# Kernel tuning notes

Measured on AMD Instinct MI355X. Metric: run time of the kernel, lower is better.

Reference implementation:

```python
import jax, jax.numpy as jnp
import numpy as np

VOCAB, EMB, HID, L = 100000, 128, 256, 9
B, S = 128, 512
H = HID // 2  # per-direction hidden size
PAD = 0


def setup_inputs() -> dict:
    key = jax.random.key(0)
    ks = jax.random.split(key, 18)
    seqs = jax.random.randint(ks[0], (B, S), 1, VOCAB)
    # left-aligned padding: lengths in [S//2, S]
    lens = jax.random.randint(ks[1], (B,), S // 2, S + 1)
    seqs = jnp.where(jnp.arange(S)[None, :] < lens[:, None], seqs, PAD)
    labels = jax.random.randint(ks[2], (B, S), 0, L)

    def n(k, shape, s=0.05):
        return jax.random.normal(k, shape, jnp.float32) * s

    emb = n(ks[3], (VOCAB, EMB)).at[PAD].set(0.0)
    inp = {
        'sequences': seqs, 'labels': labels, 'emb': emb,
        'w_ih_f': n(ks[4], (4 * H, EMB)), 'w_hh_f': n(ks[5], (4 * H, H)),
        'b_ih_f': n(ks[6], (4 * H,)), 'b_hh_f': n(ks[7], (4 * H,)),
        'w_ih_b': n(ks[8], (4 * H, EMB)), 'w_hh_b': n(ks[9], (4 * H, H)),
        'b_ih_b': n(ks[10], (4 * H,)), 'b_hh_b': n(ks[11], (4 * H,)),
        'w_out': n(ks[12], (L, HID)), 'b_out': n(ks[13], (L,)),
        'start_t': n(ks[14], (L,), 0.1), 'end_t': n(ks[15], (L,), 0.1),
        'trans': n(ks[16], (L, L), 0.1),
    }
    return inp


def _lstm_scan(x, w_ih, w_hh, b_ih, b_hh):
    # x: [S, B, E] -> hidden states [S, B, H]
    h0 = jnp.zeros((x.shape[1], w_hh.shape[1]), x.dtype)

    def step(carry, xt):
        h, c = carry
        g = xt @ w_ih.T + b_ih + h @ w_hh.T + b_hh
        i, f, gg, o = jnp.split(g, 4, axis=-1)  # PyTorch gate order i,f,g,o
        c = jax.nn.sigmoid(f) * c + jax.nn.sigmoid(i) * jnp.tanh(gg)
        h = jax.nn.sigmoid(o) * jnp.tanh(c)
        return (h, c), h

    _, hs = jax.lax.scan(step, (h0, h0), x)
    return hs


def reference(sequences, labels, emb, w_ih_f, w_hh_f, b_ih_f, b_hh_f,
              w_ih_b, w_hh_b, b_ih_b, b_hh_b, w_out, b_out,
              start_t, end_t, trans):
    # Embedding lookup (dropout is identity at inference)
    x = emb[sequences]                      # [B,S,E]
    xt = jnp.swapaxes(x, 0, 1)              # [S,B,E]
    hf = _lstm_scan(xt, w_ih_f, w_hh_f, b_ih_f, b_hh_f)
    hb = _lstm_scan(xt[::-1], w_ih_b, w_hh_b, b_ih_b, b_hh_b)[::-1]
    hcat = jnp.concatenate([hf, hb], axis=-1)         # [S,B,HID]
    emissions = jnp.swapaxes(hcat, 0, 1) @ w_out.T + b_out  # [B,S,L]

    mask = sequences != PAD                 # [B,S], first step all True
    maskf = mask.astype(emissions.dtype)

    # --- CRF numerator (score of gold path) ---
    em_tag = jnp.take_along_axis(emissions, labels[..., None], axis=2)[..., 0]  # [B,S]
    trans_sc = trans[labels[:, :-1], labels[:, 1:]]                              # [B,S-1]
    num = start_t[labels[:, 0]] + em_tag[:, 0] \
        + jnp.sum((trans_sc + em_tag[:, 1:]) * maskf[:, 1:], axis=1)
    seq_ends = jnp.sum(mask, axis=1) - 1
    last_tags = labels[jnp.arange(labels.shape[0]), seq_ends]
    num = num + end_t[last_tags]

    # --- CRF partition function (forward algorithm) ---
    def fstep(score, inp):
        em_t, m_t = inp  # [B,L], [B]
        nxt = jax.nn.logsumexp(score[:, :, None] + trans[None] + em_t[:, None, :], axis=1)
        return jnp.where(m_t[:, None], nxt, score), None

    score0 = start_t[None, :] + emissions[:, 0]  # [B,L]
    em_rest = jnp.swapaxes(emissions, 0, 1)[1:]  # [S-1,B,L]
    scoreT, _ = jax.lax.scan(fstep, score0, (em_rest, mask.T[1:]))
    denom = jax.nn.logsumexp(scoreT + end_t[None, :], axis=1)  # [B]

    # model returns -log_likelihood (torchcrf default reduction='sum')
    return -jnp.sum(num - denom)
```

## Files before the change

### kernel.cpp

```cpp
#include <hip/hip_runtime.h>
#include <hip/hip_bf16.h>

#define B_   128
#define S_   512
#define H_   128
#define G_   512
#define EMB_ 128
#define NL_  9

typedef __attribute__((ext_vector_type(8))) short bf16x8;
typedef __attribute__((ext_vector_type(4))) short bf16x4;
typedef __attribute__((ext_vector_type(4))) float f32x4;
typedef unsigned short ushort_t;

__device__ __forceinline__ void wg_bar() {
    asm volatile("s_waitcnt lgkmcnt(0)\n\ts_barrier" ::: "memory");
}

__device__ __forceinline__ float bfbits2f(short s) {
    unsigned int u = ((unsigned int)(unsigned short)s) << 16;
    return __builtin_bit_cast(float, u);
}
__device__ __forceinline__ short f2bf(float f) {
    unsigned int u = __builtin_bit_cast(unsigned int, f);
    u += 0x7FFFu + ((u >> 16) & 1u);
    return (short)(u >> 16);
}
__device__ __forceinline__ unsigned int pack2(float lo, float hi) {
    return (unsigned int)(unsigned short)f2bf(lo) | ((unsigned int)(unsigned short)f2bf(hi) << 16);
}
__device__ __forceinline__ float exp2_(float x) {
    float r;
    asm("v_exp_f32 %0, %1" : "=v"(r) : "v"(x));
    return r;
}
__device__ __forceinline__ float sigm(float x) {
    return __builtin_amdgcn_rcpf(1.f + exp2_(-1.4426950408889634f * x));
}
__device__ __forceinline__ float tanh_(float x) {
    return 1.f - 2.f * __builtin_amdgcn_rcpf(1.f + exp2_(2.8853900817779268f * x));
}

__global__ __launch_bounds__(512, 1)
void xw_gemm_kernel(const int* __restrict__ seq, const float* __restrict__ emb,
                    const float* __restrict__ w_ih_f, const float* __restrict__ b_ih_f,
                    const float* __restrict__ b_hh_f,
                    const float* __restrict__ w_ih_b, const float* __restrict__ b_ih_b,
                    const float* __restrict__ b_hh_b,
                    ushort_t* __restrict__ xw)
{
    __shared__ bf16x8 ldsX[64 * 17];

    const int tid  = threadIdx.x;
    const int wv   = tid >> 6;
    const int n16  = tid & 15;
    const int quad = (tid & 63) >> 4;
    const int dir  = blockIdx.x >> 10;
    const int rem  = blockIdx.x & 1023;
    const int pair = rem >> 4;
    const int tb   = (rem & 15) * 32;

    const float* wih = dir ? w_ih_b : w_ih_f;
    const float* bih = dir ? b_ih_b : b_ih_f;
    const float* bhh = dir ? b_hh_b : b_hh_f;

    {
        int row = tid >> 3, part = tid & 7;
        int b = 2 * pair + (row >> 5);
        int t = tb + (row & 31);
        int tok = seq[b * S_ + t];
        const float* ep = emb + (size_t)tok * EMB_ + part * 16;
        int rt = row >> 4, rr = row & 15;
#pragma unroll
        for (int h = 0; h < 2; h++) {
            float4 a = *(const float4*)(ep + h * 8);
            float4 b4 = *(const float4*)(ep + h * 8 + 4);
            bf16x8 fr;
            fr[0] = f2bf(a.x); fr[1] = f2bf(a.y); fr[2] = f2bf(a.z); fr[3] = f2bf(a.w);
            fr[4] = f2bf(b4.x); fr[5] = f2bf(b4.y); fr[6] = f2bf(b4.z); fr[7] = f2bf(b4.w);
            ldsX[(rt * 16 + part * 2 + h) * 17 + rr] = fr;
        }
    }

    bf16x8 bfrag[4][4];
    float  bias[4];
#pragma unroll
    for (int nt = 0; nt < 4; nt++) {
        int col = nt * 128 + wv * 16 + n16;
        bias[nt] = bih[col] + bhh[col];
#pragma unroll
        for (int ks = 0; ks < 4; ks++) {
            const float* p = wih + col * EMB_ + ks * 32 + quad * 8;
            bf16x8 fr;
#pragma unroll
            for (int j = 0; j < 8; j++) fr[j] = f2bf(p[j]);
            bfrag[nt][ks] = fr;
        }
    }
    __syncthreads();

    const size_t plane0 = (size_t)(dir * 128 + 2 * pair);

#pragma unroll
    for (int half = 0; half < 2; half++) {
        f32x4 accA[4], accB[4];
        bf16x8 afA[4], afB[4];
#pragma unroll
        for (int ks = 0; ks < 4; ks++) {
            afA[ks] = ldsX[(half * 16 + ks * 4 + quad) * 17 + n16];
            afB[ks] = ldsX[((half + 2) * 16 + ks * 4 + quad) * 17 + n16];
        }
#pragma unroll
        for (int nt = 0; nt < 4; nt++) {
            f32x4 a = {bias[nt], bias[nt], bias[nt], bias[nt]};
            accA[nt] = a; accB[nt] = a;
#pragma unroll
            for (int ks = 0; ks < 4; ks++) {
                accA[nt] = __builtin_amdgcn_mfma_f32_16x16x32_bf16(afA[ks], bfrag[nt][ks], accA[nt], 0, 0, 0);
                accB[nt] = __builtin_amdgcn_mfma_f32_16x16x32_bf16(afB[ks], bfrag[nt][ks], accB[nt], 0, 0, 0);
            }
        }
        const int u = wv * 16 + n16;
#pragma unroll
        for (int r = 0; r < 4; r++) {
            int t = tb + half * 16 + quad * 4 + r;
            int2 iv0, iv1;
            iv0.x = (int)pack2(accA[0][r], accA[1][r]);
            iv0.y = (int)pack2(accA[2][r], accA[3][r]);
            iv1.x = (int)pack2(accB[0][r], accB[1][r]);
            iv1.y = (int)pack2(accB[2][r], accB[3][r]);
            *(int2*)(xw + ((plane0 * S_ + t) * 128 + u) * 4) = iv0;
            *(int2*)(xw + (((plane0 + 1) * S_ + t) * 128 + u) * 4) = iv1;
        }
    }
}

#define STEPK(k)                                                                   \
  {                                                                                \
    if ((k) == 0 && s4 == 0 && m < 31) {                                           \
      const ushort_t* gp = xwp + (size_t)(dir ? (S_ - 32 - m16) : (m16 + 16)) * 512; \
      sA = *(const int4*)(gp + tid * 8);                                           \
      sB = *(const int4*)(gp + 2048 + tid * 8);                                    \
      sC = *(const int4*)(gp + 4096 + tid * 8);                                    \
      sD = *(const int4*)(gp + 6144 + tid * 8);                                    \
    }                                                                              \
    bf16x8 af0 = hbuf[(k) & 1][0 * 4 + quad];                                      \
    bf16x8 af1 = hbuf[(k) & 1][1 * 4 + quad];                                      \
    bf16x8 af2 = hbuf[(k) & 1][2 * 4 + quad];                                      \
    bf16x8 af3 = hbuf[(k) & 1][3 * 4 + quad];                                      \
    const int KE = s4x4 + (k);                                                     \
    const int slot = dir ? (15 - KE) : KE;                                         \
    bf16x4 xvg = *(const bf16x4*)(xwS + (m & 1) * 8192 + slot * 512 + uu * 4);     \
    if ((k) == 0 && s4 == 2 && m < 31) {                                           \
      int4* dst = (int4*)(xwL + (((m & 1) ^ 1) * 1024));                           \
      dst[tid] = sA; dst[256 + tid] = sB; dst[512 + tid] = sC; dst[768 + tid] = sD; \
    }                                                                              \
    if ((k) == 1 && s4 == 0 && m >= 1 && wv == 3 && lane < 36) {                   \
      int a0 = dir ? (S_ - m16) : (m16 - 16);                                      \
      float4 fv = *(const float4*)(emL + (a0 & 31) * 9 + lane * 4);                \
      *(float4*)(emdir + (size_t)b * (S_ * NL_) + a0 * NL_ + lane * 4) = fv;       \
    }                                                                              \
    f32x4 aA0 = __builtin_amdgcn_mfma_f32_16x16x32_bf16(af0, bfrag[0][0][0], ZACC, 0, 0, 0); \
    f32x4 aA1 = __builtin_amdgcn_mfma_f32_16x16x32_bf16(af0, bfrag[0][1][0], ZACC, 0, 0, 0); \
    f32x4 aA2 = __builtin_amdgcn_mfma_f32_16x16x32_bf16(af0, bfrag[0][2][0], ZACC, 0, 0, 0); \
    f32x4 aA3 = __builtin_amdgcn_mfma_f32_16x16x32_bf16(af0, bfrag[0][3][0], ZACC, 0, 0, 0); \
    f32x4 aB0 = __builtin_amdgcn_mfma_f32_16x16x32_bf16(af0, bfrag[1][0][0], ZACC, 0, 0, 0); \
    f32x4 aB1 = __builtin_amdgcn_mfma_f32_16x16x32_bf16(af0, bfrag[1][1][0], ZACC, 0, 0, 0); \
    f32x4 aB2 = __builtin_amdgcn_mfma_f32_16x16x32_bf16(af0, bfrag[1][2][0], ZACC, 0, 0, 0); \
    f32x4 aB3 = __builtin_amdgcn_mfma_f32_16x16x32_bf16(af0, bfrag[1][3][0], ZACC, 0, 0, 0); \
    aA0 = __builtin_amdgcn_mfma_f32_16x16x32_bf16(af1, bfrag[0][0][1], aA0, 0, 0, 0); \
    aA1 = __builtin_amdgcn_mfma_f32_16x16x32_bf16(af1, bfrag[0][1][1], aA1, 0, 0, 0); \
    aA2 = __builtin_amdgcn_mfma_f32_16x16x32_bf16(af1, bfrag[0][2][1], aA2, 0, 0, 0); \
    aA3 = __builtin_amdgcn_mfma_f32_16x16x32_bf16(af1, bfrag[0][3][1], aA3, 0, 0, 0); \
    aB0 = __builtin_amdgcn_mfma_f32_16x16x32_bf16(af1, bfrag[1][0][1], aB0, 0, 0, 0); \
    aB1 = __builtin_amdgcn_mfma_f32_16x16x32_bf16(af1, bfrag[1][1][1], aB1, 0, 0, 0); \
    aB2 = __builtin_amdgcn_mfma_f32_16x16x32_bf16(af1, bfrag[1][2][1], aB2, 0, 0, 0); \
    aB3 = __builtin_amdgcn_mfma_f32_16x16x32_bf16(af1, bfrag[1][3][1], aB3, 0, 0, 0); \
    aA0 = __builtin_amdgcn_mfma_f32_16x16x32_bf16(af2, bfrag[0][0][2], aA0, 0, 0, 0); \
    aA1 = __builtin_amdgcn_mfma_f32_16x16x32_bf16(af2, bfrag[0][1][2], aA1, 0, 0, 0); \
    aA2 = __builtin_amdgcn_mfma_f32_16x16x32_bf16(af2, bfrag[0][2][2], aA2, 0, 0, 0); \
    aA3 = __builtin_amdgcn_mfma_f32_16x16x32_bf16(af2, bfrag[0][3][2], aA3, 0, 0, 0); \
    aB0 = __builtin_amdgcn_mfma_f32_16x16x32_bf16(af2, bfrag[1][0][2], aB0, 0, 0, 0); \
    aB1 = __builtin_amdgcn_mfma_f32_16x16x32_bf16(af2, bfrag[1][1][2], aB1, 0, 0, 0); \
    aB2 = __builtin_amdgcn_mfma_f32_16x16x32_bf16(af2, bfrag[1][2][2], aB2, 0, 0, 0); \
    aB3 = __builtin_amdgcn_mfma_f32_16x16x32_bf16(af2, bfrag[1][3][2], aB3, 0, 0, 0); \
    aA0 = __builtin_amdgcn_mfma_f32_16x16x32_bf16(af3, bfrag[0][0][3], aA0, 0, 0, 0); \
    aA1 = __builtin_amdgcn_mfma_f32_16x16x32_bf16(af3, bfrag[0][1][3], aA1, 0, 0, 0); \
    aA2 = __builtin_amdgcn_mfma_f32_16x16x32_bf16(af3, bfrag[0][2][3], aA2, 0, 0, 0); \
    aA3 = __builtin_amdgcn_mfma_f32_16x16x32_bf16(af3, bfrag[0][3][3], aA3, 0, 0, 0); \
    aB0 = __builtin_amdgcn_mfma_f32_16x16x32_bf16(af3, bfrag[1][0][3], aB0, 0, 0, 0); \
    aB1 = __builtin_amdgcn_mfma_f32_16x16x32_bf16(af3, bfrag[1][1][3], aB1, 0, 0, 0); \
    aB2 = __builtin_amdgcn_mfma_f32_16x16x32_bf16(af3, bfrag[1][2][3], aB2, 0, 0, 0); \
    aB3 = __builtin_amdgcn_mfma_f32_16x16x32_bf16(af3, bfrag[1][3][3], aB3, 0, 0, 0); \
    {                                                                              \
      float gi = ((quad & 2) ? aB0[0] : aA0[0]) + bfbits2f(xvg[0]);                \
      float gf = ((quad & 2) ? aB1[0] : aA1[0]) + bfbits2f(xvg[1]);                \
      float gg = ((quad & 2) ? aB2[0] : aA2[0]) + bfbits2f(xvg[2]);                \
      float go = ((quad & 2) ? aB3[0] : aA3[0]) + bfbits2f(xvg[3]);                \
      float Af = exp2_(-1.4426950408889634f * gf);                                 \
      float Bi = exp2_(-1.4426950408889634f * gi);                                 \
      float Cg = exp2_(2.8853900817779268f * gg);                                  \
      float Fo = exp2_(-1.4426950408889634f * go);                                 \
      float oA = 1.f + Af, oB = 1.f + Bi, oC = 1.f + Cg;                           \
      float P = oB * oC;                                                           \
      float numer = cst * P + oA * (Cg - 1.f);                                     \
      cst = numer * __builtin_amdgcn_rcpf(oA * P);                                 \
      float hv = tanh_(cst) * __builtin_amdgcn_rcpf(1.f + Fo);                     \
      if (!(quad & 1)) *(((k) & 1) ? hw0 : hw1) = f2bf(hv);                        \
    }                                                                              \
    if (wv == 0) {                                                                 \
      f32x4 accE = __builtin_amdgcn_mfma_f32_16x16x32_bf16(af0, bfragE[0], ZACC, 0, 0, 0); \
      accE = __builtin_amdgcn_mfma_f32_16x16x32_bf16(af1, bfragE[1], accE, 0, 0, 0); \
      accE = __builtin_amdgcn_mfma_f32_16x16x32_bf16(af2, bfragE[2], accE, 0, 0, 0); \
      accE = __builtin_amdgcn_mfma_f32_16x16x32_bf16(af3, bfragE[3], accE, 0, 0, 0); \
      if (quad == 0 && n16 < NL_ && (m16 + KE) >= 1) {                             \
        int tprev = dir ? (S_ - (m16 + KE)) : (m16 + KE - 1);                      \
        emL[(tprev & 31) * 9 + n16] = accE[0];                                     \
      }                                                                            \
    }                                                                              \
    wg_bar();                                                                      \
  }

__global__ __launch_bounds__(256, 1)
void lstm_kernel(const ushort_t* __restrict__ xw,
                 const float* __restrict__ w_hh_f, const float* __restrict__ w_hh_b,
                 const float* __restrict__ w_out,
                 float* __restrict__ em_f, float* __restrict__ em_b)
{
    __shared__ bf16x8 xwL[2 * 1024];
    __shared__ bf16x8 hbuf[2][16];
    __shared__ __align__(16) float emL[32 * NL_];

    const int tid  = threadIdx.x;
    const int wv   = tid >> 6;
    const int lane = tid & 63;
    const int n16  = tid & 15;
    const int quad = (tid & 63) >> 4;
    const int dir  = blockIdx.x >> 7;
    const int b    = blockIdx.x & 127;

    const int uu = wv * 32 + ((quad >> 1) << 4) + n16;

    short* hw0 = ((short*)hbuf) + uu;
    short* hw1 = ((short*)hbuf) + 128 + uu;
    const short* xwS = (const short*)xwL;

    const f32x4 ZACC = {0.f, 0.f, 0.f, 0.f};

    const float* whh = dir ? w_hh_b : w_hh_f;
    float* emdir = dir ? em_b : em_f;

    bf16x8 bfrag[2][4][4];
#pragma unroll
    for (int tl = 0; tl < 2; tl++) {
#pragma unroll
        for (int nt = 0; nt < 4; nt++) {
            int col = nt * 128 + wv * 32 + tl * 16 + n16;
#pragma unroll
            for (int ks = 0; ks < 4; ks++) {
                const float* p = whh + col * H_ + ks * 32 + quad * 8;
                bf16x8 fr;
#pragma unroll
                for (int j = 0; j < 8; j++) fr[j] = f2bf(p[j]);
                bfrag[tl][nt][ks] = fr;
            }
        }
    }
    bf16x8 bfragE[4];
#pragma unroll
    for (int ks = 0; ks < 4; ks++) {
        bf16x8 fr = {0, 0, 0, 0, 0, 0, 0, 0};
        if (n16 < NL_) {
            const float* p = w_out + n16 * 256 + dir * 128 + ks * 32 + quad * 8;
#pragma unroll
            for (int j = 0; j < 8; j++) fr[j] = f2bf(p[j]);
        }
        bfragE[ks] = fr;
    }

    if (tid < 64) ((int*)hbuf)[tid] = 0;

    const ushort_t* xwp = xw + (size_t)(dir * 128 + b) * ((size_t)S_ * 512);
    {
        const ushort_t* gp = xwp + (size_t)(dir ? (S_ - 16) : 0) * 512;
        int4 a0 = *(const int4*)(gp + tid * 8);
        int4 a1 = *(const int4*)(gp + 2048 + tid * 8);
        int4 a2 = *(const int4*)(gp + 4096 + tid * 8);
        int4 a3 = *(const int4*)(gp + 6144 + tid * 8);
        int4* dst = (int4*)xwL;
        dst[tid] = a0; dst[256 + tid] = a1; dst[512 + tid] = a2; dst[768 + tid] = a3;
    }

    float cst = 0.f;
    int4 sA, sB, sC, sD;
    wg_bar();

#pragma unroll 1
    for (int m = 0; m < 32; m++) {
        const int m16 = m << 4;
#pragma unroll 1
        for (int s4 = 0; s4 < 4; s4++) {
            const int s4x4 = s4 << 2;
            STEPK(0) STEPK(1) STEPK(2) STEPK(3)
        }
    }

    if (wv == 0) {
        bf16x8 af0 = hbuf[0][0 * 4 + quad];
        bf16x8 af1 = hbuf[0][1 * 4 + quad];
        bf16x8 af2 = hbuf[0][2 * 4 + quad];
        bf16x8 af3 = hbuf[0][3 * 4 + quad];
        f32x4 accE = __builtin_amdgcn_mfma_f32_16x16x32_bf16(af0, bfragE[0], ZACC, 0, 0, 0);
        accE = __builtin_amdgcn_mfma_f32_16x16x32_bf16(af1, bfragE[1], accE, 0, 0, 0);
        accE = __builtin_amdgcn_mfma_f32_16x16x32_bf16(af2, bfragE[2], accE, 0, 0, 0);
        accE = __builtin_amdgcn_mfma_f32_16x16x32_bf16(af3, bfragE[3], accE, 0, 0, 0);
        if (quad == 0 && n16 < NL_) {
            int tprev = dir ? 0 : (S_ - 1);
            emL[(tprev & 31) * 9 + n16] = accE[0];
        }
    }
    wg_bar();
    if (wv == 3 && lane < 36) {
        int a0 = dir ? 0 : (S_ - 16);
        float4 fv = *(const float4*)(emL + (a0 & 31) * 9 + lane * 4);
        *(float4*)(emdir + (size_t)b * (S_ * NL_) + a0 * NL_ + lane * 4) = fv;
    }
}

__global__ __launch_bounds__(640, 1)
void crf_kernel(const int* __restrict__ seq, const int* __restrict__ lab,
                const float* __restrict__ em_f, const float* __restrict__ em_b,
                const float* __restrict__ b_out,
                const float* __restrict__ start_t, const float* __restrict__ end_t,
                const float* __restrict__ trans, float* __restrict__ partial)
{
    __shared__ float emS[S_ * NL_];
    __shared__ float transS[NL_ * NL_];
    __shared__ float stS[NL_], enS[NL_];
    __shared__ unsigned char maskS[S_];
    __shared__ float MS[7 * 81];
    __shared__ float vS[NL_];
    __shared__ float redw[10];
    __shared__ int   redl[10];

    const int b = blockIdx.x, tid = threadIdx.x;
    const size_t base = (size_t)b * S_ * NL_;
    const float L2E = 1.4426950408889634f, LN2 = 0.6931471805599453f;

    for (int q = tid; q < S_ * NL_; q += 640)
        emS[q] = em_f[base + q] + em_b[base + q] + b_out[q % NL_];
    if (tid < NL_ * NL_) transS[tid] = trans[tid];
    if (tid < NL_) { stS[tid] = start_t[tid]; enS[tid] = end_t[tid]; }
    if (tid < S_) maskS[tid] = (seq[b * S_ + tid] != 0);
    __syncthreads();

    float np = 0.f; int myc = 0;
    if (tid < S_) {
        myc = maskS[tid];
        if (tid >= 1 && maskS[tid]) {
            int lp = lab[b * S_ + tid - 1], lc = lab[b * S_ + tid];
            np = transS[lp * NL_ + lc] + emS[tid * NL_ + lc];
        }
    }
#pragma unroll
    for (int off = 32; off; off >>= 1) {
        np  += __shfl_down(np, off, 64);
        myc += __shfl_down(myc, off, 64);
    }
    if ((tid & 63) == 0) { redw[tid >> 6] = np; redl[tid >> 6] = myc; }

    const int w = tid >> 6, l = tid & 63;
    const int lg = l / 9;
    const int g  = w * 7 + lg;
    const bool sact = (lg < 7) && (g < 64);
    const int jj = sact ? (l - lg * 9) : 0;
    const int gb = sact ? lg * 9 : 0;
    float Tc[NL_];
#pragma unroll
    for (int i = 0; i < NL_; i++) Tc[i] = transS[i * NL_ + jj];
    float sc; int tbeg, tend, cN = 0, iN = 0;
    if (sact && g == 0) {
        sc = stS[jj] + emS[jj];
        tbeg = 1; tend = 64;
    } else if (sact) {
        cN = 1 + (g - 1) / 9; iN = (g - 1) % 9;
        sc = (jj == iN) ? 0.f : -1e30f;
        tbeg = cN * 64; tend = tbeg + 64;
    } else {
        sc = -1e30f; tbeg = 448; tend = 512;
    }
    for (int t = tbeg; t < tend; t++) {
        float emv = emS[t * NL_ + jj];
        float a[NL_];
#pragma unroll
        for (int i = 0; i < NL_; i++) a[i] = __shfl(sc, gb + i, 64) + Tc[i];
        float m = a[0];
#pragma unroll
        for (int i = 1; i < NL_; i++) m = fmaxf(m, a[i]);
        float sum = 0.f;
#pragma unroll
        for (int i = 0; i < NL_; i++) sum += exp2f((a[i] - m) * L2E);
        float nxt = emv + m + LN2 * log2f(sum);
        sc = maskS[t] ? nxt : sc;
    }
    if (sact) {
        if (g == 0) vS[jj] = sc;
        else MS[(cN - 1) * 81 + iN * NL_ + jj] = sc;
    }
    __syncthreads();

    if (tid < 64) {
        const int j = (tid < NL_) ? tid : (NL_ - 1);
        float v = vS[j];
        for (int c = 1; c < 8; c++) {
            float a[NL_];
#pragma unroll
            for (int i = 0; i < NL_; i++)
                a[i] = __shfl(v, i, 64) + MS[(c - 1) * 81 + i * NL_ + j];
            float m = a[0];
#pragma unroll
            for (int i = 1; i < NL_; i++) m = fmaxf(m, a[i]);
            float sum = 0.f;
#pragma unroll
            for (int i = 0; i < NL_; i++) sum += exp2f((a[i] - m) * L2E);
            v = m + LN2 * log2f(sum);
        }
        v += enS[j];
        float mm = -1e30f, av[NL_];
#pragma unroll
        for (int i = 0; i < NL_; i++) { float vi = __shfl(v, i, 64); av[i] = vi; mm = fmaxf(mm, vi); }
        float ss = 0.f;
#pragma unroll
        for (int i = 0; i < NL_; i++) ss += exp2f((av[i] - mm) * L2E);
        if (tid == 0) {
            float num = 0.f; int len = 0;
#pragma unroll
            for (int ww = 0; ww < 10; ww++) { num += redw[ww]; len += redl[ww]; }
            int l0 = lab[b * S_];
            int ll = lab[b * S_ + len - 1];
            num += stS[l0] + emS[l0] + enS[ll];
            partial[b] = (mm + LN2 * log2f(ss)) - num;
        }
    }
}

__global__ __launch_bounds__(128)
void reduce_kernel(const float* __restrict__ partial, float* __restrict__ out)
{
    __shared__ float s[128];
    int tid = threadIdx.x;
    s[tid] = partial[tid];
    __syncthreads();
    for (int off = 64; off; off >>= 1) {
        if (tid < off) s[tid] += s[tid + off];
        __syncthreads();
    }
    if (tid == 0) out[0] = s[0];
}

extern "C" void kernel_launch(void* const* d_in, const int* in_sizes, int n_in,
                              void* d_out, int out_size, void* d_ws, size_t ws_size,
                              hipStream_t stream)
{
    const int* seq = (const int*)d_in[0];
    const int* lab = (const int*)d_in[1];
    const float* emb    = (const float*)d_in[2];
    const float* w_ih_f = (const float*)d_in[3];
    const float* w_hh_f = (const float*)d_in[4];
    const float* b_ih_f = (const float*)d_in[5];
    const float* b_hh_f = (const float*)d_in[6];
    const float* w_ih_b = (const float*)d_in[7];
    const float* w_hh_b = (const float*)d_in[8];
    const float* b_ih_b = (const float*)d_in[9];
    const float* b_hh_b = (const float*)d_in[10];
    const float* w_out  = (const float*)d_in[11];
    const float* b_out  = (const float*)d_in[12];
    const float* start_t = (const float*)d_in[13];
    const float* end_t   = (const float*)d_in[14];
    const float* trans   = (const float*)d_in[15];

    char* ws = (char*)d_ws;
    const size_t xw_bytes = (size_t)2 * B_ * S_ * G_ * sizeof(ushort_t);
    const size_t em_bytes = (size_t)B_ * S_ * NL_ * sizeof(float);
    ushort_t* xw   = (ushort_t*)ws;
    float* em_f    = (float*)(ws + xw_bytes);
    float* em_b    = (float*)(ws + xw_bytes + em_bytes);
    float* partial = (float*)(ws + xw_bytes + 2 * em_bytes);

    xw_gemm_kernel<<<dim3(2048), dim3(512), 0, stream>>>(seq, emb,
        w_ih_f, b_ih_f, b_hh_f, w_ih_b, b_ih_b, b_hh_b, xw);
    lstm_kernel<<<dim3(256), dim3(256), 0, stream>>>(xw, w_hh_f, w_hh_b,
        w_out, em_f, em_b);
    crf_kernel<<<dim3(B_), dim3(640), 0, stream>>>(seq, lab, em_f, em_b, b_out,
        start_t, end_t, trans, partial);
    reduce_kernel<<<dim3(1), dim3(128), 0, stream>>>(partial, (float*)d_out);
}
```

Before: 497.4 us.

## Fuse input-projection GEMM into LSTM recurrence kernel, drop xw workspace

Removes the separate xw_gemm kernel and its large bf16 workspace. Each LSTM workgroup now gathers the embeddings for the next 16 timesteps, converts them to bf16 and runs a small MFMA GEMM against register-resident W_ih fragments, writing into the LDS staging buffer in the slots of the recurrence steps. This cuts the global write and read of the input-projection tensor and one launch. The cost is many more registers held across the recurrent loop and extra MFMA work on the serial critical path. The CRF logsumexp also switches to v_max3, raw v_exp/v_log and tree sums.

```diff
diff --git a/kernel.cpp b/kernel.cpp
--- a/kernel.cpp
+++ b/kernel.cpp
@@ -30,119 +30,64 @@
     return (unsigned int)(unsigned short)f2bf(lo) | ((unsigned int)(unsigned short)f2bf(hi) << 16);
 }
 __device__ __forceinline__ float exp2_(float x) {
-    float r;
-    asm("v_exp_f32 %0, %1" : "=v"(r) : "v"(x));
-    return r;
-}
-__device__ __forceinline__ float sigm(float x) {
-    return __builtin_amdgcn_rcpf(1.f + exp2_(-1.4426950408889634f * x));
+    float r; asm("v_exp_f32 %0, %1" : "=v"(r) : "v"(x)); return r;
+}
+__device__ __forceinline__ float log2_(float x) {
+    float r; asm("v_log_f32 %0, %1" : "=v"(r) : "v"(x)); return r;
+}
+__device__ __forceinline__ float max3_(float a, float b, float c) {
+    float r; asm("v_max3_f32 %0, %1, %2, %3" : "=v"(r) : "v"(a), "v"(b), "v"(c)); return r;
 }
 __device__ __forceinline__ float tanh_(float x) {
     return 1.f - 2.f * __builtin_amdgcn_rcpf(1.f + exp2_(2.8853900817779268f * x));
 }
-
-__global__ __launch_bounds__(512, 1)
-void xw_gemm_kernel(const int* __restrict__ seq, const float* __restrict__ emb,
-                    const float* __restrict__ w_ih_f, const float* __restrict__ b_ih_f,
-                    const float* __restrict__ b_hh_f,
-                    const float* __restrict__ w_ih_b, const float* __restrict__ b_ih_b,
-                    const float* __restrict__ b_hh_b,
-                    ushort_t* __restrict__ xw)
-{
-    __shared__ bf16x8 ldsX[64 * 17];
-
-    const int tid  = threadIdx.x;
-    const int wv   = tid >> 6;
-    const int n16  = tid & 15;
-    const int quad = (tid & 63) >> 4;
-    const int dir  = blockIdx.x >> 10;
-    const int rem  = blockIdx.x & 1023;
-    const int pair = rem >> 4;
-    const int tb   = (rem & 15) * 32;
-
-    const float* wih = dir ? w_ih_b : w_ih_f;
-    const float* bih = dir ? b_ih_b : b_ih_f;
-    const float* bhh = dir ? b_hh_b : b_hh_f;
-
-    {
-        int row = tid >> 3, part = tid & 7;
-        int b = 2 * pair + (row >> 5);
-        int t = tb + (row & 31);
-        int tok = seq[b * S_ + t];
-        const float* ep = emb + (size_t)tok * EMB_ + part * 16;
-        int rt = row >> 4, rr = row & 15;
-#pragma unroll
-        for (int h = 0; h < 2; h++) {
-            float4 a = *(const float4*)(ep + h * 8);
-            float4 b4 = *(const float4*)(ep + h * 8 + 4);
-            bf16x8 fr;
-            fr[0] = f2bf(a.x); fr[1] = f2bf(a.y); fr[2] = f2bf(a.z); fr[3] = f2bf(a.w);
-            fr[4] = f2bf(b4.x); fr[5] = f2bf(b4.y); fr[6] = f2bf(b4.z); fr[7] = f2bf(b4.w);
-            ldsX[(rt * 16 + part * 2 + h) * 17 + rr] = fr;
-        }
-    }
-
-    bf16x8 bfrag[4][4];
-    float  bias[4];
-#pragma unroll
-    for (int nt = 0; nt < 4; nt++) {
-        int col = nt * 128 + wv * 16 + n16;
-        bias[nt] = bih[col] + bhh[col];
-#pragma unroll
-        for (int ks = 0; ks < 4; ks++) {
-            const float* p = wih + col * EMB_ + ks * 32 + quad * 8;
-            bf16x8 fr;
-#pragma unroll
-            for (int j = 0; j < 8; j++) fr[j] = f2bf(p[j]);
-            bfrag[nt][ks] = fr;
-        }
-    }
-    __syncthreads();
-
-    const size_t plane0 = (size_t)(dir * 128 + 2 * pair);
-
-#pragma unroll
-    for (int half = 0; half < 2; half++) {
-        f32x4 accA[4], accB[4];
-        bf16x8 afA[4], afB[4];
-#pragma unroll
-        for (int ks = 0; ks < 4; ks++) {
-            afA[ks] = ldsX[(half * 16 + ks * 4 + quad) * 17 + n16];
-            afB[ks] = ldsX[((half + 2) * 16 + ks * 4 + quad) * 17 + n16];
-        }
-#pragma unroll
-        for (int nt = 0; nt < 4; nt++) {
-            f32x4 a = {bias[nt], bias[nt], bias[nt], bias[nt]};
-            accA[nt] = a; accB[nt] = a;
-#pragma unroll
-            for (int ks = 0; ks < 4; ks++) {
-                accA[nt] = __builtin_amdgcn_mfma_f32_16x16x32_bf16(afA[ks], bfrag[nt][ks], accA[nt], 0, 0, 0);
-                accB[nt] = __builtin_amdgcn_mfma_f32_16x16x32_bf16(afB[ks], bfrag[nt][ks], accB[nt], 0, 0, 0);
-            }
-        }
-        const int u = wv * 16 + n16;
-#pragma unroll
-        for (int r = 0; r < 4; r++) {
-            int t = tb + half * 16 + quad * 4 + r;
-            int2 iv0, iv1;
-            iv0.x = (int)pack2(accA[0][r], accA[1][r]);
-            iv0.y = (int)pack2(accA[2][r], accA[3][r]);
-            iv1.x = (int)pack2(accB[0][r], accB[1][r]);
-            iv1.y = (int)pack2(accB[2][r], accB[3][r]);
-            *(int2*)(xw + ((plane0 * S_ + t) * 128 + u) * 4) = iv0;
-            *(int2*)(xw + (((plane0 + 1) * S_ + t) * 128 + u) * 4) = iv1;
-        }
-    }
-}
+__device__ __forceinline__ bf16x8 cvt8(float4 a, float4 b) {
+    bf16x8 r;
+    r[0] = f2bf(a.x); r[1] = f2bf(a.y); r[2] = f2bf(a.z); r[3] = f2bf(a.w);
+    r[4] = f2bf(b.x); r[5] = f2bf(b.y); r[6] = f2bf(b.z); r[7] = f2bf(b.w);
+    return r;
+}
+
+#define MINIGEMM(tl, bufsel)                                                       \
+    {                                                                              \
+      f32x4 x0 = {biasI[tl][0], biasI[tl][0], biasI[tl][0], biasI[tl][0]};         \
+      f32x4 x1 = {biasI[tl][1], biasI[tl][1], biasI[tl][1], biasI[tl][1]};         \
+      f32x4 x2 = {biasI[tl][2], biasI[tl][2], biasI[tl][2], biasI[tl][2]};         \
+      f32x4 x3 = {biasI[tl][3], biasI[tl][3], biasI[tl][3], biasI[tl][3]};         \
+      x0 = __builtin_amdgcn_mfma_f32_16x16x32_bf16(afE0, bfragI[tl][0][0], x0, 0, 0, 0); \
+      x1 = __builtin_amdgcn_mfma_f32_16x16x32_bf16(afE0, bfragI[tl][1][0], x1, 0, 0, 0); \
+      x2 = __builtin_amdgcn_mfma_f32_16x16x32_bf16(afE0, bfragI[tl][2][0], x2, 0, 0, 0); \
+      x3 = __builtin_amdgcn_mfma_f32_16x16x32_bf16(afE0, bfragI[tl][3][0], x3, 0, 0, 0); \
+      x0 = __builtin_amdgcn_mfma_f32_16x16x32_bf16(afE1, bfragI[tl][0][1], x0, 0, 0, 0); \
+      x1 = __builtin_amdgcn_mfma_f32_16x16x32_bf16(afE1, bfragI[tl][1][1], x1, 0, 0, 0); \
+      x2 = __builtin_amdgcn_mfma_f32_16x16x32_bf16(afE1, bfragI[tl][2][1], x2, 0, 0, 0); \
+      x3 = __builtin_amdgcn_mfma_f32_16x16x32_bf16(afE1, bfragI[tl][3][1], x3, 0, 0, 0); \
+      x0 = __builtin_amdgcn_mfma_f32_16x16x32_bf16(afE2, bfragI[tl][0][2], x0, 0, 0, 0); \
+      x1 = __builtin_amdgcn_mfma_f32_16x16x32_bf16(afE2, bfragI[tl][1][2], x1, 0, 0, 0); \
+      x2 = __builtin_amdgcn_mfma_f32_16x16x32_bf16(afE2, bfragI[tl][2][2], x2, 0, 0, 0); \
+      x3 = __builtin_amdgcn_mfma_f32_16x16x32_bf16(afE2, bfragI[tl][3][2], x3, 0, 0, 0); \
+      x0 = __builtin_amdgcn_mfma_f32_16x16x32_bf16(afE3, bfragI[tl][0][3], x0, 0, 0, 0); \
+      x1 = __builtin_amdgcn_mfma_f32_16x16x32_bf16(afE3, bfragI[tl][1][3], x1, 0, 0, 0); \
+      x2 = __builtin_amdgcn_mfma_f32_16x16x32_bf16(afE3, bfragI[tl][2][3], x2, 0, 0, 0); \
+      x3 = __builtin_amdgcn_mfma_f32_16x16x32_bf16(afE3, bfragI[tl][3][3], x3, 0, 0, 0); \
+      short* dstp = xwSW + (bufsel) * 8192 + (wv * 32 + (tl) * 16 + n16) * 4;      \
+      _Pragma("unroll")                                                            \
+      for (int r = 0; r < 4; r++) {                                                \
+        uint2 wq; wq.x = pack2(x0[r], x1[r]); wq.y = pack2(x2[r], x3[r]);          \
+        *(uint2*)(dstp + (quad * 4 + r) * 512) = wq;                               \
+      }                                                                            \
+    }
 
 #define STEPK(k)                                                                   \
   {                                                                                \
     if ((k) == 0 && s4 == 0 && m < 31) {                                           \
-      const ushort_t* gp = xwp + (size_t)(dir ? (S_ - 32 - m16) : (m16 + 16)) * 512; \
-      sA = *(const int4*)(gp + tid * 8);                                           \
-      sB = *(const int4*)(gp + 2048 + tid * 8);                                    \
-      sC = *(const int4*)(gp + 4096 + tid * 8);                                    \
-      sD = *(const int4*)(gp + 6144 + tid * 8);                                    \
+      int t0s = dir ? (S_ - 32 - m16) : (m16 + 16);                                \
+      int tok = seq[b * S_ + t0s + n16];                                           \
+      const float* ep = emb + (size_t)tok * EMB_ + quad * 8;                       \
+      e0 = *(const float4*)(ep);        e1 = *(const float4*)(ep + 4);             \
+      e2 = *(const float4*)(ep + 32);   e3 = *(const float4*)(ep + 36);            \
+      e4 = *(const float4*)(ep + 64);   e5 = *(const float4*)(ep + 68);            \
+      e6 = *(const float4*)(ep + 96);   e7 = *(const float4*)(ep + 100);           \
     }                                                                              \
     bf16x8 af0 = hbuf[(k) & 1][0 * 4 + quad];                                      \
     bf16x8 af1 = hbuf[(k) & 1][1 * 4 + quad];                                      \
@@ -151,10 +96,10 @@
     const int KE = s4x4 + (k);                                                     \
     const int slot = dir ? (15 - KE) : KE;                                         \
     bf16x4 xvg = *(const bf16x4*)(xwS + (m & 1) * 8192 + slot * 512 + uu * 4);     \
-    if ((k) == 0 && s4 == 2 && m < 31) {                                           \
-      int4* dst = (int4*)(xwL + (((m & 1) ^ 1) * 1024));                           \
-      dst[tid] = sA; dst[256 + tid] = sB; dst[512 + tid] = sC; dst[768 + tid] = sD; \
-    }                                                                              \
+    if ((k) == 0 && s4 == 1 && m < 31) { afE0 = cvt8(e0, e1); afE1 = cvt8(e2, e3); } \
+    if ((k) == 2 && s4 == 1 && m < 31) { afE2 = cvt8(e4, e5); afE3 = cvt8(e6, e7); } \
+    if ((k) == 0 && s4 == 2 && m < 31) MINIGEMM(0, ((m & 1) ^ 1))                  \
+    if ((k) == 2 && s4 == 2 && m < 31) MINIGEMM(1, ((m & 1) ^ 1))                  \
     if ((k) == 1 && s4 == 0 && m >= 1 && wv == 3 && lane < 36) {                   \
       int a0 = dir ? (S_ - m16) : (m16 - 16);                                      \
       float4 fv = *(const float4*)(emL + (a0 & 31) * 9 + lane * 4);                \
@@ -222,7 +167,11 @@
   }
 
 __global__ __launch_bounds__(256, 1)
-void lstm_kernel(const ushort_t* __restrict__ xw,
+void lstm_kernel(const int* __restrict__ seq, const float* __restrict__ emb,
+                 const float* __restrict__ w_ih_f, const float* __restrict__ b_ih_f,
+                 const float* __restrict__ b_hh_f,
+                 const float* __restrict__ w_ih_b, const float* __restrict__ b_ih_b,
+                 const float* __restrict__ b_hh_b,
                  const float* __restrict__ w_hh_f, const float* __restrict__ w_hh_b,
                  const float* __restrict__ w_out,
                  float* __restrict__ em_f, float* __restrict__ em_b)
@@ -244,10 +193,14 @@
     short* hw0 = ((short*)hbuf) + uu;
     short* hw1 = ((short*)hbuf) + 128 + uu;
     const short* xwS = (const short*)xwL;
+    short* xwSW = (short*)xwL;
 
     const f32x4 ZACC = {0.f, 0.f, 0.f, 0.f};
 
     const float* whh = dir ? w_hh_b : w_hh_f;
+    const float* wih = dir ? w_ih_b : w_ih_f;
+    const float* bih = dir ? b_ih_b : b_ih_f;
+    const float* bhh = dir ? b_hh_b : b_hh_f;
     float* emdir = dir ? em_b : em_f;
 
     bf16x8 bfrag[2][4][4];
@@ -263,6 +216,24 @@
 #pragma unroll
                 for (int j = 0; j < 8; j++) fr[j] = f2bf(p[j]);
                 bfrag[tl][nt][ks] = fr;
+            }
+        }
+    }
+    bf16x8 bfragI[2][4][4];
+    float  biasI[2][4];
+#pragma unroll
+    for (int tl = 0; tl < 2; tl++) {
+#pragma unroll
+        for (int nt = 0; nt < 4; nt++) {
+            int col = nt * 128 + wv * 32 + tl * 16 + n16;
+            biasI[tl][nt] = bih[col] + bhh[col];
+#pragma unroll
+            for (int ks = 0; ks < 4; ks++) {
+                const float* p = wih + col * EMB_ + ks * 32 + quad * 8;
+                bf16x8 fr;
+#pragma unroll
+                for (int j = 0; j < 8; j++) fr[j] = f2bf(p[j]);
+                bfragI[tl][nt][ks] = fr;
             }
         }
     }
@@ -280,19 +251,24 @@
 
     if (tid < 64) ((int*)hbuf)[tid] = 0;
 
-    const ushort_t* xwp = xw + (size_t)(dir * 128 + b) * ((size_t)S_ * 512);
+    float4 e0, e1, e2, e3, e4, e5, e6, e7;
+    bf16x8 afE0, afE1, afE2, afE3;
+
     {
-        const ushort_t* gp = xwp + (size_t)(dir ? (S_ - 16) : 0) * 512;
-        int4 a0 = *(const int4*)(gp + tid * 8);
-        int4 a1 = *(const int4*)(gp + 2048 + tid * 8);
-        int4 a2 = *(const int4*)(gp + 4096 + tid * 8);
-        int4 a3 = *(const int4*)(gp + 6144 + tid * 8);
-        int4* dst = (int4*)xwL;
-        dst[tid] = a0; dst[256 + tid] = a1; dst[512 + tid] = a2; dst[768 + tid] = a3;
+        int t0s = dir ? (S_ - 16) : 0;
+        int tok = seq[b * S_ + t0s + n16];
+        const float* ep = emb + (size_t)tok * EMB_ + quad * 8;
+        e0 = *(const float4*)(ep);        e1 = *(const float4*)(ep + 4);
+        e2 = *(const float4*)(ep + 32);   e3 = *(const float4*)(ep + 36);
+        e4 = *(const float4*)(ep + 64);   e5 = *(const float4*)(ep + 68);
+        e6 = *(const float4*)(ep + 96);   e7 = *(const float4*)(ep + 100);
+        afE0 = cvt8(e0, e1); afE1 = cvt8(e2, e3);
+        afE2 = cvt8(e4, e5); afE3 = cvt8(e6, e7);
+        MINIGEMM(0, 0)
+        MINIGEMM(1, 0)
     }
 
     float cst = 0.f;
-    int4 sA, sB, sC, sD;
     wg_bar();
 
 #pragma unroll 1
@@ -394,13 +370,13 @@
         float a[NL_];
 #pragma unroll
         for (int i = 0; i < NL_; i++) a[i] = __shfl(sc, gb + i, 64) + Tc[i];
-        float m = a[0];
-#pragma unroll
-        for (int i = 1; i < NL_; i++) m = fmaxf(m, a[i]);
-        float sum = 0.f;
-#pragma unroll
-        for (int i = 0; i < NL_; i++) sum += exp2f((a[i] - m) * L2E);
-        float nxt = emv + m + LN2 * log2f(sum);
+        float m = max3_(max3_(a[0], a[1], a[2]), max3_(a[3], a[4], a[5]),
+                        max3_(a[6], a[7], a[8]));
+        float e[NL_];
+#pragma unroll
+        for (int i = 0; i < NL_; i++) e[i] = exp2_((a[i] - m) * L2E);
+        float sum = ((e[0] + e[1]) + (e[2] + e[3])) + ((e[4] + e[5]) + (e[6] + e[7])) + e[8];
+        float nxt = emv + m + LN2 * log2_(sum);
         sc = maskS[t] ? nxt : sc;
     }
     if (sact) {
@@ -417,13 +393,13 @@
 #pragma unroll
             for (int i = 0; i < NL_; i++)
                 a[i] = __shfl(v, i, 64) + MS[(c - 1) * 81 + i * NL_ + j];
-            float m = a[0];
-#pragma unroll
-            for (int i = 1; i < NL_; i++) m = fmaxf(m, a[i]);
-            float sum = 0.f;
-#pragma unroll
-            for (int i = 0; i < NL_; i++) sum += exp2f((a[i] - m) * L2E);
-            v = m + LN2 * log2f(sum);
+            float m = max3_(max3_(a[0], a[1], a[2]), max3_(a[3], a[4], a[5]),
+                            max3_(a[6], a[7], a[8]));
+            float e[NL_];
+#pragma unroll
+            for (int i = 0; i < NL_; i++) e[i] = exp2_((a[i] - m) * L2E);
+            float sum = ((e[0] + e[1]) + (e[2] + e[3])) + ((e[4] + e[5]) + (e[6] + e[7])) + e[8];
+            v = m + LN2 * log2_(sum);
         }
         v += enS[j];
         float mm = -1e30f, av[NL_];
@@ -431,7 +407,7 @@
         for (int i = 0; i < NL_; i++) { float vi = __shfl(v, i, 64); av[i] = vi; mm = fmaxf(mm, vi); }
         float ss = 0.f;
 #pragma unroll
-        for (int i = 0; i < NL_; i++) ss += exp2f((av[i] - mm) * L2E);
+        for (int i = 0; i < NL_; i++) ss += exp2_((av[i] - mm) * L2E);
         if (tid == 0) {
             float num = 0.f; int len = 0;
 #pragma unroll
@@ -439,7 +415,7 @@
             int l0 = lab[b * S_];
             int ll = lab[b * S_ + len - 1];
             num += stS[l0] + emS[l0] + enS[ll];
-            partial[b] = (mm + LN2 * log2f(ss)) - num;
+            partial[b] = (mm + LN2 * log2_(ss)) - num;
         }
     }
 }
@@ -480,17 +456,14 @@
     const float* trans   = (const float*)d_in[15];
 
     char* ws = (char*)d_ws;
-    const size_t xw_bytes = (size_t)2 * B_ * S_ * G_ * sizeof(ushort_t);
     const size_t em_bytes = (size_t)B_ * S_ * NL_ * sizeof(float);
-    ushort_t* xw   = (ushort_t*)ws;
-    float* em_f    = (float*)(ws + xw_bytes);
-    float* em_b    = (float*)(ws + xw_bytes + em_bytes);
-    float* partial = (float*)(ws + xw_bytes + 2 * em_bytes);
-
-    xw_gemm_kernel<<<dim3(2048), dim3(512), 0, stream>>>(seq, emb,
-        w_ih_f, b_ih_f, b_hh_f, w_ih_b, b_ih_b, b_hh_b, xw);
-    lstm_kernel<<<dim3(256), dim3(256), 0, stream>>>(xw, w_hh_f, w_hh_b,
-        w_out, em_f, em_b);
+    float* em_f    = (float*)ws;
+    float* em_b    = (float*)(ws + em_bytes);
+    float* partial = (float*)(ws + 2 * em_bytes);
+
+    lstm_kernel<<<dim3(256), dim3(256), 0, stream>>>(seq, emb,
+        w_ih_f, b_ih_f, b_hh_f, w_ih_b, b_ih_b, b_hh_b,
+        w_hh_f, w_hh_b, w_out, em_f, em_b);
     crf_kernel<<<dim3(B_), dim3(640), 0, stream>>>(seq, lab, em_f, em_b, b_out,
         start_t, end_t, trans, partial);
     reduce_kernel<<<dim3(1), dim3(128), 0, stream>>>(partial, (float*)d_out);
```

After: 513.9 us. 1.03x slower.
